# Kernel optimization log

Hardware: AMD Instinct MI355X
Metric: run time of the kernel (lower is better)

Reference implementation:

```python
import jax, jax.numpy as jnp
import numpy as np

N_AB = 8
L = 3
N_REF = 3
ANC = 0
M = 20
NV = N_AB
NQ = N_AB + N_REF + ANC  # 11
K = N_AB - L             # 5
DIM = 2 ** NQ            # 2048

# CNOT as (in_c, in_t, out_c, out_t); matches einsum 'bvf,fg->bvg' with f=(q1,q2) bits
CNOT4 = jnp.array([[1., 0, 0, 0],
                   [0, 1, 0, 0],
                   [0, 0, 0, 1],
                   [0, 0, 1, 0]], dtype=jnp.float32).reshape(2, 2, 2, 2)


def ry_mat(angle):
    c = jnp.cos(angle / 2.0)
    s = jnp.sin(angle / 2.0)
    # [[c, -s], [s, c]]; original contracts as state @ gate ('bvi,ij->bvj')
    return jnp.stack([jnp.stack([c, -s]), jnp.stack([s, c])])


def apply_1q(state, q, gate):
    # state: [b, 2^NQ]; qubit q is big-endian axis q of [2]*NQ view
    b = state.shape[0]
    t = state.reshape(b, 2 ** q, 2, -1)
    out = jnp.einsum('blir,ij->bljr', t, gate)
    return out.reshape(b, -1)


def apply_2q(state, q1, q2, gate4):
    # gate4: [2,2,2,2] with indices (in_q1, in_q2, out_q1, out_q2)
    b = state.shape[0]
    a, c = (q1, q2) if q1 < q2 else (q2, q1)
    t = state.reshape(b, 2 ** a, 2, 2 ** (c - a - 1), 2, -1)
    if q1 < q2:
        out = jnp.einsum('bxiyjz,ijkl->bxkylz', t, gate4)
    else:
        out = jnp.einsum('bxjyiz,ijkl->bxlykz', t, gate4)
    return out.reshape(b, -1)


def setup_inputs() -> dict:
    key = jax.random.key(0)
    k1, k2 = jax.random.split(key)
    x = jax.random.uniform(k1, (1024, 2 ** N_AB), dtype=jnp.float32)
    theta = jax.random.normal(k2, ((M + 1) * NV,), dtype=jnp.float32) * 0.08
    return {"x": x, "theta": theta}


def reference(x, theta):
    b = x.shape[0]
    # amplitude encode: state[:, i << (n_ref+anc)] = x[:, i]
    inds = np.arange(2 ** N_AB) << (N_REF + ANC)
    state = jnp.zeros((b, DIM), dtype=x.dtype).at[:, inds].set(x)
    pidx = 0
    for m in range(M):
        for q in range(NV):
            state = apply_1q(state, q, ry_mat(theta[pidx + q]))
        pidx += NV
        # cw_fixed ring: control q -> target (q+1) % NV
        for q in range(NV):
            state = apply_2q(state, q, (q + 1) % NV, CNOT4)
    for q in range(NV):
        state = apply_1q(state, q, ry_mat(theta[pidx + q]))
    # qubits: A = 0..K-1, B = K..K+L-1, Bp = rest (anc=0)
    t = state.reshape(b, 2 ** K, 2 ** L, 2 ** N_REF)
    probs_B = jnp.sum(t * t, axis=(1, 3))  # [b, 2^L]
    return probs_B
```

## Files before the change

kernel.cpp:

```cpp
#include <hip/hip_runtime.h>


#define N_ANGLES 168

__device__ __forceinline__ void ry_layer(int lane, const float* __restrict__ tb,
                                         float& s0, float& s1, float& s2, float& s3) {
    #pragma unroll
    for (int q = 0; q < 6; ++q) {
        const float cv = tb[2 * q];
        const float sv = tb[2 * q + 1];
        const int lb = 5 - q;
        const int mask = 1 << lb;
        const float sg = ((lane >> lb) & 1) ? -sv : sv;
        const float p0 = __shfl_xor(s0, mask);
        const float p1 = __shfl_xor(s1, mask);
        const float p2 = __shfl_xor(s2, mask);
        const float p3 = __shfl_xor(s3, mask);
        s0 = cv * s0 + sg * p0;
        s1 = cv * s1 + sg * p1;
        s2 = cv * s2 + sg * p2;
        s3 = cv * s3 + sg * p3;
    }
    {
        const float cv = tb[12], sv = tb[13];
        const float n0 = cv * s0 + sv * s2;
        const float n2 = cv * s2 - sv * s0;
        const float n1 = cv * s1 + sv * s3;
        const float n3 = cv * s3 - sv * s1;
        s0 = n0; s1 = n1; s2 = n2; s3 = n3;
    }
    {
        const float cv = tb[14], sv = tb[15];
        const float n0 = cv * s0 + sv * s1;
        const float n1 = cv * s1 - sv * s0;
        const float n2 = cv * s2 + sv * s3;
        const float n3 = cv * s3 - sv * s2;
        s0 = n0; s1 = n1; s2 = n2; s3 = n3;
    }
}

__global__ __launch_bounds__(256) void qae_kernel(const float* __restrict__ x,
                                                  const float* __restrict__ theta,
                                                  float* __restrict__ out) {
    __shared__ float tab[N_ANGLES * 2];
    const int t = threadIdx.x;
    if (t < N_ANGLES) {
        const float a = theta[t] * 0.5f;
        tab[2 * t]     = cosf(a);
        tab[2 * t + 1] = sinf(a);
    }
    __syncthreads();

    const int lane = t & 63;
    const int wave = t >> 6;
    const int b = blockIdx.x * 4 + wave;

    const float4 xv = *reinterpret_cast<const float4*>(x + (size_t)b * 256 + lane * 4);
    float s0 = xv.x, s1 = xv.y, s2 = xv.z, s3 = xv.w;

    #pragma unroll
    for (int m = 0; m < 20; ++m) {
        const float* tb = &tab[m * 16];
        ry_layer(lane, tb, s0, s1, s2, s3);

        #pragma unroll
        for (int q = 0; q < 5; ++q) {
            const int cb = 5 - q;
            const int tmask = 1 << (4 - q);
            const bool cond = (lane >> cb) & 1;
            const float p0 = __shfl_xor(s0, tmask);
            const float p1 = __shfl_xor(s1, tmask);
            const float p2 = __shfl_xor(s2, tmask);
            const float p3 = __shfl_xor(s3, tmask);
            s0 = cond ? p0 : s0;
            s1 = cond ? p1 : s1;
            s2 = cond ? p2 : s2;
            s3 = cond ? p3 : s3;
        }
        {
            const bool cond = lane & 1;
            const float t0 = s0, t1 = s1;
            s0 = cond ? s2 : s0;
            s2 = cond ? t0 : s2;
            s1 = cond ? s3 : s1;
            s3 = cond ? t1 : s3;
        }
        {
            const float tt = s2; s2 = s3; s3 = tt;
        }
        s1 = __shfl_xor(s1, 32);
        s3 = __shfl_xor(s3, 32);
    }

    ry_layer(lane, &tab[320], s0, s1, s2, s3);

    float p0 = s0 * s0, p1 = s1 * s1, p2 = s2 * s2, p3 = s3 * s3;
    #pragma unroll
    for (int m = 2; m <= 32; m <<= 1) {
        p0 += __shfl_xor(p0, m);
        p1 += __shfl_xor(p1, m);
        p2 += __shfl_xor(p2, m);
        p3 += __shfl_xor(p3, m);
    }
    if (lane < 2) {
        *reinterpret_cast<float4*>(out + (size_t)b * 8 + lane * 4) =
            make_float4(p0, p1, p2, p3);
    }
}

extern "C" void kernel_launch(void* const* d_in, const int* in_sizes, int n_in,
                              void* d_out, int out_size, void* d_ws, size_t ws_size,
                              hipStream_t stream) {
    const float* x = (const float*)d_in[0];
    const float* theta = (const float*)d_in[1];
    float* out = (float*)d_out;

    qae_kernel<<<256, 256, 0, stream>>>(x, theta, out);
}
```

Before: 19.61 us.

## Eliminate CNOT ring permutations by tracking GF(2) basis transform at compile time

Replaces the explicit CNOT-ring permutation shuffles with a compile-time GF(2) linear-map tracking of the cumulative CNOT transform. Each RY pair is applied in a transformed basis as a fused two-qubit stage using precomputed cos/sin products. The final measurement bins probabilities through the tracked map. This removes the per-layer permutation shuffles and halves the rotation stages. In exchange, each stage now needs up to three shuffle-sourced operands plus popcount-based sign logic, and the final reduction covers eight accumulators instead of four.

```diff
diff --git a/kernel.cpp b/kernel.cpp
--- a/kernel.cpp
+++ b/kernel.cpp
@@ -1,119 +1,169 @@
 #include <hip/hip_runtime.h>
 
 
-#define N_ANGLES 168
+namespace {
 
-__device__ __forceinline__ void ry_layer(int lane, const float* __restrict__ tb,
-                                         float& s0, float& s1, float& s2, float& s3) {
-    #pragma unroll
-    for (int q = 0; q < 6; ++q) {
-        const float cv = tb[2 * q];
-        const float sv = tb[2 * q + 1];
-        const int lb = 5 - q;
-        const int mask = 1 << lb;
-        const float sg = ((lane >> lb) & 1) ? -sv : sv;
-        const float p0 = __shfl_xor(s0, mask);
-        const float p1 = __shfl_xor(s1, mask);
-        const float p2 = __shfl_xor(s2, mask);
-        const float p3 = __shfl_xor(s3, mask);
-        s0 = cv * s0 + sg * p0;
-        s1 = cv * s1 + sg * p1;
-        s2 = cv * s2 + sg * p2;
-        s3 = cv * s3 + sg * p3;
+struct M8 { unsigned r[8]; };
+
+constexpr M8 kI{{0x01,0x02,0x04,0x08,0x10,0x20,0x40,0x80}};
+constexpr M8 kP{{0xFF,0xFE,0xFC,0xF8,0xF0,0xE0,0xC0,0x7F}};
+constexpr M8 kQ{{0x03,0x06,0x0C,0x18,0x30,0x60,0xC1,0x81}};
+
+constexpr M8 mul(const M8& A, const M8& B) {
+  M8 C{{0,0,0,0,0,0,0,0}};
+  for (int j = 0; j < 8; ++j) {
+    unsigned by = 0;
+    for (int b = 0; b < 8; ++b) by |= ((B.r[b] >> j) & 1u) << b;
+    for (int b = 0; b < 8; ++b) {
+      unsigned v = A.r[b] & by;
+      v ^= v >> 4; v ^= v >> 2; v ^= v >> 1;
+      C.r[b] |= (v & 1u) << j;
     }
-    {
-        const float cv = tb[12], sv = tb[13];
-        const float n0 = cv * s0 + sv * s2;
-        const float n2 = cv * s2 - sv * s0;
-        const float n1 = cv * s1 + sv * s3;
-        const float n3 = cv * s3 - sv * s1;
-        s0 = n0; s1 = n1; s2 = n2; s3 = n3;
+  }
+  return C;
+}
+
+constexpr bool eqI(const M8& A) {
+  bool e = true;
+  for (int b = 0; b < 8; ++b) e = e && (A.r[b] == (1u << b));
+  return e;
+}
+
+struct Tables { unsigned Mm[21][8]; unsigned Rr[21][8]; bool ok; };
+
+constexpr Tables build() {
+  Tables t{};
+  M8 T = kI, Ti = kI;
+  bool ok = eqI(mul(kP, kQ)) && eqI(mul(kQ, kP));
+  for (int m = 0; m <= 20; ++m) {
+    ok = ok && eqI(mul(T, Ti));
+    for (int b = 0; b < 8; ++b) {
+      unsigned mm = 0;
+      for (int k = 0; k < 8; ++k) mm |= ((Ti.r[k] >> b) & 1u) << k;
+      t.Mm[m][b] = mm;
+      t.Rr[m][b] = T.r[b];
     }
-    {
-        const float cv = tb[14], sv = tb[15];
-        const float n0 = cv * s0 + sv * s1;
-        const float n1 = cv * s1 - sv * s0;
-        const float n2 = cv * s2 + sv * s3;
-        const float n3 = cv * s3 - sv * s2;
-        s0 = n0; s1 = n1; s2 = n2; s3 = n3;
-    }
+    T = mul(kP, T);
+    Ti = mul(Ti, kQ);
+  }
+  t.ok = ok;
+  return t;
+}
+
+constexpr Tables kT = build();
+static_assert(kT.ok, "GF(2) inverse tracking failed");
+static_assert(kT.Mm[0][5] == 0x20 && kT.Rr[0][3] == 0x08, "layer-0 must be identity");
+
+template<unsigned M, int J>
+__device__ __forceinline__ float part(const float (&s)[4]) {
+  constexpr int jj = J ^ (int)(M & 3u);
+  constexpr int lm = (int)(M >> 2);
+  float v = s[jj];
+  if constexpr (lm != 0) v = __shfl_xor(v, lm);
+  return v;
+}
+
+template<int m, int st>
+__device__ __forceinline__ void stage(int lane, const float4* __restrict__ ct4, float (&s)[4]) {
+  constexpr int bA = 2 * st + 1, bB = 2 * st;
+  constexpr unsigned MA = kT.Mm[m][bA];
+  constexpr unsigned MB = kT.Mm[m][bB];
+  constexpr unsigned MC = MA ^ MB;
+  constexpr unsigned RA = kT.Rr[m][bA];
+  constexpr unsigned RB = kT.Rr[m][bB];
+
+  const float4 k = ct4[m * 4 + st];
+  const int sa = (__popc((int)(RA >> 2) & lane) & 1) << 31;
+  const int sb = (__popc((int)(RB >> 2) & lane) & 1) << 31;
+
+  float A[4] = { part<MA,0>(s), part<MA,1>(s), part<MA,2>(s), part<MA,3>(s) };
+  float B[4] = { part<MB,0>(s), part<MB,1>(s), part<MB,2>(s), part<MB,3>(s) };
+  float C[4] = { part<MC,0>(s), part<MC,1>(s), part<MC,2>(s), part<MC,3>(s) };
+
+  float ns[4];
+  #pragma unroll
+  for (int j = 0; j < 4; ++j) {
+    const int ka = ((__popc((int)(RA & 3u) & j) & 1) << 31) ^ sa;
+    const int kb = ((__popc((int)(RB & 3u) & j) & 1) << 31) ^ sb;
+    const float wa = __int_as_float(__float_as_int(k.y) ^ ka);
+    const float wb = __int_as_float(__float_as_int(k.z) ^ kb);
+    const float wc = __int_as_float(__float_as_int(k.w) ^ ka ^ kb);
+    ns[j] = k.x * s[j] + wa * A[j] + wb * B[j] + wc * C[j];
+  }
+  s[0] = ns[0]; s[1] = ns[1]; s[2] = ns[2]; s[3] = ns[3];
+}
+
+template<int m>
+__device__ __forceinline__ void run_layers(int lane, const float4* __restrict__ ct4, float (&s)[4]) {
+  if constexpr (m <= 20) {
+    stage<m, 0>(lane, ct4, s);
+    stage<m, 1>(lane, ct4, s);
+    stage<m, 2>(lane, ct4, s);
+    stage<m, 3>(lane, ct4, s);
+    run_layers<m + 1>(lane, ct4, s);
+  }
+}
+
 }
 
 __global__ __launch_bounds__(256) void qae_kernel(const float* __restrict__ x,
                                                   const float* __restrict__ theta,
                                                   float* __restrict__ out) {
-    __shared__ float tab[N_ANGLES * 2];
-    const int t = threadIdx.x;
-    if (t < N_ANGLES) {
-        const float a = theta[t] * 0.5f;
-        tab[2 * t]     = cosf(a);
-        tab[2 * t + 1] = sinf(a);
-    }
-    __syncthreads();
+  __shared__ float4 ct4[84];
+  const int t = threadIdx.x;
+  if (t < 84) {
+    const int m = t >> 2, st = t & 3;
+    const int qa = 6 - 2 * st;
+    const int qb = 7 - 2 * st;
+    float sA, cA, sB, cB;
+    sincosf(theta[m * 8 + qa] * 0.5f, &sA, &cA);
+    sincosf(theta[m * 8 + qb] * 0.5f, &sB, &cB);
+    ct4[t] = make_float4(cA * cB, sA * cB, cA * sB, sA * sB);
+  }
+  __syncthreads();
 
-    const int lane = t & 63;
-    const int wave = t >> 6;
-    const int b = blockIdx.x * 4 + wave;
+  const int lane = t & 63;
+  const int b = blockIdx.x * 4 + (t >> 6);
 
-    const float4 xv = *reinterpret_cast<const float4*>(x + (size_t)b * 256 + lane * 4);
-    float s0 = xv.x, s1 = xv.y, s2 = xv.z, s3 = xv.w;
+  const float4 xv = *reinterpret_cast<const float4*>(x + (size_t)b * 256 + lane * 4);
+  float s[4] = { xv.x, xv.y, xv.z, xv.w };
 
+  run_layers<0>(lane, ct4, s);
+
+  constexpr unsigned R0 = kT.Rr[20][0], R1 = kT.Rr[20][1], R2 = kT.Rr[20][2];
+  const int q0 = __popc((int)(R0 >> 2) & lane) & 1;
+  const int q1 = __popc((int)(R1 >> 2) & lane) & 1;
+  const int q2 = __popc((int)(R2 >> 2) & lane) & 1;
+
+  float acc[8];
+  #pragma unroll
+  for (int B = 0; B < 8; ++B) acc[B] = 0.f;
+  #pragma unroll
+  for (int j = 0; j < 4; ++j) {
+    const int bj = (q0 ^ (__popc((int)(R0 & 3u) & j) & 1))
+                 | ((q1 ^ (__popc((int)(R1 & 3u) & j) & 1)) << 1)
+                 | ((q2 ^ (__popc((int)(R2 & 3u) & j) & 1)) << 2);
+    const float pj = s[j] * s[j];
     #pragma unroll
-    for (int m = 0; m < 20; ++m) {
-        const float* tb = &tab[m * 16];
-        ry_layer(lane, tb, s0, s1, s2, s3);
-
-        #pragma unroll
-        for (int q = 0; q < 5; ++q) {
-            const int cb = 5 - q;
-            const int tmask = 1 << (4 - q);
-            const bool cond = (lane >> cb) & 1;
-            const float p0 = __shfl_xor(s0, tmask);
-            const float p1 = __shfl_xor(s1, tmask);
-            const float p2 = __shfl_xor(s2, tmask);
-            const float p3 = __shfl_xor(s3, tmask);
-            s0 = cond ? p0 : s0;
-            s1 = cond ? p1 : s1;
-            s2 = cond ? p2 : s2;
-            s3 = cond ? p3 : s3;
-        }
-        {
-            const bool cond = lane & 1;
-            const float t0 = s0, t1 = s1;
-            s0 = cond ? s2 : s0;
-            s2 = cond ? t0 : s2;
-            s1 = cond ? s3 : s1;
-            s3 = cond ? t1 : s3;
-        }
-        {
-            const float tt = s2; s2 = s3; s3 = tt;
-        }
-        s1 = __shfl_xor(s1, 32);
-        s3 = __shfl_xor(s3, 32);
-    }
-
-    ry_layer(lane, &tab[320], s0, s1, s2, s3);
-
-    float p0 = s0 * s0, p1 = s1 * s1, p2 = s2 * s2, p3 = s3 * s3;
+    for (int B = 0; B < 8; ++B) acc[B] += (bj == B) ? pj : 0.f;
+  }
+  #pragma unroll
+  for (int mm = 1; mm < 64; mm <<= 1) {
     #pragma unroll
-    for (int m = 2; m <= 32; m <<= 1) {
-        p0 += __shfl_xor(p0, m);
-        p1 += __shfl_xor(p1, m);
-        p2 += __shfl_xor(p2, m);
-        p3 += __shfl_xor(p3, m);
-    }
-    if (lane < 2) {
-        *reinterpret_cast<float4*>(out + (size_t)b * 8 + lane * 4) =
-            make_float4(p0, p1, p2, p3);
-    }
+    for (int B = 0; B < 8; ++B) acc[B] += __shfl_xor(acc[B], mm);
+  }
+  if (lane == 0) {
+    float4* o = reinterpret_cast<float4*>(out + (size_t)b * 8);
+    o[0] = make_float4(acc[0], acc[1], acc[2], acc[3]);
+    o[1] = make_float4(acc[4], acc[5], acc[6], acc[7]);
+  }
 }
 
 extern "C" void kernel_launch(void* const* d_in, const int* in_sizes, int n_in,
                               void* d_out, int out_size, void* d_ws, size_t ws_size,
                               hipStream_t stream) {
-    const float* x = (const float*)d_in[0];
-    const float* theta = (const float*)d_in[1];
-    float* out = (float*)d_out;
-
-    qae_kernel<<<256, 256, 0, stream>>>(x, theta, out);
+  const float* x = (const float*)d_in[0];
+  const float* theta = (const float*)d_in[1];
+  float* out = (float*)d_out;
+  qae_kernel<<<256, 256, 0, stream>>>(x, theta, out);
 }
```

Result: slower. 21.14 us (+7.8%).
